# Optimization experiments

Hardware: AMD Instinct MI355X
Metric: run time of the kernel (lower is better)

Reference implementation:

```python
import jax, jax.numpy as jnp
import numpy as np

INPUT_SIZE = 1024
HIDDEN_SIZE = 1024
BATCH = 32
SEQ_LEN = 1024


def setup_inputs() -> dict:
    key = jax.random.key(0)
    k1, k2, k3, k4 = jax.random.split(key, 4)
    scale_x = 1.0 / np.sqrt(INPUT_SIZE)
    scale_h = 1.0 / np.sqrt(HIDDEN_SIZE)
    X = jax.random.normal(k1, (BATCH, SEQ_LEN, INPUT_SIZE), dtype=jnp.float32)
    W_xh = jax.random.normal(k2, (INPUT_SIZE, HIDDEN_SIZE), dtype=jnp.float32) * scale_x
    W_hh = jax.random.normal(k3, (HIDDEN_SIZE, HIDDEN_SIZE), dtype=jnp.float32) * scale_h
    b_h = jax.random.normal(k4, (HIDDEN_SIZE,), dtype=jnp.float32) * 0.01
    return {"X": X, "W_xh": W_xh, "W_hh": W_hh, "b_h": b_h}


def reference(X, W_xh, W_hh, b_h):
    # Elman RNN: H_t = tanh(X_t @ W_xh + H_{t-1} @ W_hh + b)
    B, S, _ = X.shape
    H0 = jnp.zeros((B, W_hh.shape[0]), dtype=X.dtype)
    # Precompute input projection for all timesteps in one big GEMM.
    Xp = jnp.einsum('bsi,ih->bsh', X, W_xh) + b_h  # [B, S, H]

    def step(H, xp_t):
        H_new = jnp.tanh(xp_t + H @ W_hh)
        return H_new, H_new

    H_last, outs = jax.lax.scan(step, H0, jnp.swapaxes(Xp, 0, 1))  # outs: [S, B, H]
    out = jnp.swapaxes(outs, 0, 1)  # [B, S, H]
    return out, H_last
```

## Files before the change

kernel.cpp:

```cpp
#include <hip/hip_runtime.h>
#include <hip/hip_bf16.h>
#include <math.h>


#define B_SZ 32
#define S_SZ 1024
#define H_SZ 1024
#define K_SZ 1024

#define BM 128
#define BN 128
#define BK 8

__global__ __launch_bounds__(256) void proj_gemm(
    const float* __restrict__ A,
    const float* __restrict__ Bm,
    const float* __restrict__ bias,
    float* __restrict__ C,
    int M, int N, int K)
{
    __shared__ float As[BK][BM];
    __shared__ float Bs[BK][BN];

    const int tid  = threadIdx.x;
    const int row0 = blockIdx.y * BM;
    const int col0 = blockIdx.x * BN;
    const int tx = tid & 15;
    const int ty = tid >> 4;
    const int mBase = ty * 8;
    const int nBase = tx * 8;

    float acc[8][8];
    #pragma unroll
    for (int i = 0; i < 8; ++i)
        #pragma unroll
        for (int j = 0; j < 8; ++j) acc[i][j] = 0.f;

    for (int k0 = 0; k0 < K; k0 += BK) {
        {
            const int r  = tid >> 1;
            const int kq = (tid & 1) * 4;
            const float4 av = *(const float4*)(&A[(size_t)(row0 + r) * K + k0 + kq]);
            As[kq + 0][r] = av.x;
            As[kq + 1][r] = av.y;
            As[kq + 2][r] = av.z;
            As[kq + 3][r] = av.w;
            const int kr = tid >> 5;
            const int cq = (tid & 31) * 4;
            *(float4*)(&Bs[kr][cq]) =
                *(const float4*)(&Bm[(size_t)(k0 + kr) * N + col0 + cq]);
        }
        __syncthreads();

        #pragma unroll
        for (int kk = 0; kk < BK; ++kk) {
            float a[8], b[8];
            *(float4*)&a[0] = *(const float4*)&As[kk][mBase];
            *(float4*)&a[4] = *(const float4*)&As[kk][mBase + 4];
            *(float4*)&b[0] = *(const float4*)&Bs[kk][nBase];
            *(float4*)&b[4] = *(const float4*)&Bs[kk][nBase + 4];
            #pragma unroll
            for (int i = 0; i < 8; ++i)
                #pragma unroll
                for (int j = 0; j < 8; ++j)
                    acc[i][j] += a[i] * b[j];
        }
        __syncthreads();
    }

    #pragma unroll
    for (int i = 0; i < 8; ++i) {
        const int r = row0 + mBase + i;
        #pragma unroll
        for (int jq = 0; jq < 8; jq += 4) {
            const int c = col0 + nBase + jq;
            const float4 bv = *(const float4*)(&bias[c]);
            float4 o;
            o.x = acc[i][jq + 0] + bv.x;
            o.y = acc[i][jq + 1] + bv.y;
            o.z = acc[i][jq + 2] + bv.z;
            o.w = acc[i][jq + 3] + bv.w;
            *(float4*)(&C[(size_t)r * N + c]) = o;
        }
    }
}

__global__ void init_cnt(unsigned int* __restrict__ cnt, int n) {
    int i = blockIdx.x * 256 + threadIdx.x;
    if (i < n) cnt[i] = 0u;
}

__global__ __launch_bounds__(512, 2) void rnn_persist(
    float* __restrict__ HS,
    const float* __restrict__ W,
    float* __restrict__ Hlast,
    unsigned int* __restrict__ cnt
    )
{
    const int g    = blockIdx.x & 7;
    const int c    = blockIdx.x >> 3;
    const int col0 = c * 32;
    const int b0   = g * 4;
    const int tid  = threadIdx.x;
    const int j    = tid & 31;
    const int seg  = tid >> 5;

    __shared__ __align__(16) float Hs[4][1024];
    __shared__ float red[8][4][32];

    float w[64];
    {
        const float* wp = W + (size_t)(seg * 64) * H_SZ + col0 + j;
        #pragma unroll
        for (int i = 0; i < 64; ++i) w[i] = wp[(size_t)i * H_SZ];
        #pragma unroll
        for (int i = 0; i < 64; ++i) asm volatile("" : "+v"(w[i]));
    }

    unsigned int* flag = cnt + g * S_SZ;

    for (int t = 0; t < S_SZ; ++t) {
        if (t > 0) {
            if (tid == 0) {
                while (__hip_atomic_load(flag + (t - 1), __ATOMIC_RELAXED,
                                         __HIP_MEMORY_SCOPE_AGENT) < 32u) {
                    __builtin_amdgcn_s_sleep(2);
                }
            }
            __syncthreads();

            #pragma unroll
            for (int ch = 0; ch < 4; ++ch) {
                const int f8 = tid + ch * 512;
                const int b  = f8 >> 9;
                const int qw = f8 & 511;
                const unsigned long long* src = (const unsigned long long*)
                    (&HS[((size_t)(b0 + b) * S_SZ + (t - 1)) * H_SZ]);
                const unsigned long long v8 = __hip_atomic_load(
                    &src[qw], __ATOMIC_RELAXED, __HIP_MEMORY_SCOPE_AGENT);
                *(unsigned long long*)(&Hs[b][qw * 2]) = v8;
            }
            __syncthreads();

            float acc[4];
            #pragma unroll
            for (int b = 0; b < 4; ++b) {
                const float4* hb = (const float4*)(&Hs[b][seg * 64]);
                float a = 0.f;
                #pragma unroll
                for (int q = 0; q < 16; ++q) {
                    const float4 h = hb[q];
                    a += h.x * w[4 * q + 0];
                    a += h.y * w[4 * q + 1];
                    a += h.z * w[4 * q + 2];
                    a += h.w * w[4 * q + 3];
                }
                acc[b] = a;
            }
            #pragma unroll
            for (int b = 0; b < 4; ++b) acc[b] += __shfl_xor(acc[b], 32);
            const int wv = tid >> 6;
            if ((tid & 63) < 32) {
                #pragma unroll
                for (int b = 0; b < 4; ++b) red[wv][b][j] = acc[b];
            }
            __syncthreads();
        }

        if (tid < 128) {
            const int b  = tid >> 5;
            const int jj = tid & 31;
            float s = 0.f;
            if (t > 0) {
                #pragma unroll
                for (int wv2 = 0; wv2 < 8; ++wv2) s += red[wv2][b][jj];
            }
            const size_t idx = ((size_t)(b0 + b) * S_SZ + t) * H_SZ + col0 + jj;
            const float v = tanhf(HS[idx] + s);
            __hip_atomic_store(&HS[idx], v, __ATOMIC_RELAXED,
                               __HIP_MEMORY_SCOPE_AGENT);
            if (t == S_SZ - 1)
                Hlast[(size_t)(b0 + b) * H_SZ + col0 + jj] = v;
        }

        __syncthreads();
        if (tid == 0) {
            __hip_atomic_fetch_add(flag + t, 1u, __ATOMIC_RELAXED,
                                   __HIP_MEMORY_SCOPE_AGENT);
        }
    }
}

extern "C" void kernel_launch(void* const* d_in, const int* in_sizes, int n_in,
                              void* d_out, int out_size, void* d_ws, size_t ws_size,
                              hipStream_t stream) {
    const float* X    = (const float*)d_in[0];
    const float* W_xh = (const float*)d_in[1];
    const float* W_hh = (const float*)d_in[2];
    const float* b_h  = (const float*)d_in[3];
    float* out = (float*)d_out;
    float* Hlast = out + (size_t)B_SZ * S_SZ * H_SZ;
    unsigned int* cnt = (unsigned int*)d_ws;

    init_cnt<<<(8 * S_SZ + 255) / 256, 256, 0, stream>>>(cnt, 8 * S_SZ);

    dim3 gridA(H_SZ / BN, (B_SZ * S_SZ) / BM);
    proj_gemm<<<gridA, 256, 0, stream>>>(X, W_xh, b_h, out,
                                         B_SZ * S_SZ, H_SZ, K_SZ);

    rnn_persist<<<256, 512, 0, stream>>>(out, W_hh, Hlast, cnt);
}
```

Measured before the change: 4.714 ms.

## Replace shared step counter with per-block flags polled by all threads

Replaces the per-timestep shared atomic counter with one monotonically increasing flag per producer block. Each thread polls only the flag of the block that wrote the slice it loads, so the leading thread spin plus block barrier before loading the previous hidden state goes away. The change also prefetches the input-projection values at the start of each step, uses an exp-based fast tanh, and drops one block barrier by publishing the flag right after a vmcnt wait in the writer threads. In exchange it takes on memory-ordering risk, since it relies on relaxed atomics plus s_waitcnt for visibility, and the fast tanh is slightly less accurate.

```diff
diff --git a/kernel.cpp b/kernel.cpp
--- a/kernel.cpp
+++ b/kernel.cpp
@@ -1,5 +1,4 @@
 #include <hip/hip_runtime.h>
-#include <hip/hip_bf16.h>
 #include <math.h>
 
 
@@ -88,6 +87,12 @@
 __global__ void init_cnt(unsigned int* __restrict__ cnt, int n) {
     int i = blockIdx.x * 256 + threadIdx.x;
     if (i < n) cnt[i] = 0u;
+}
+
+__device__ __forceinline__ float fast_tanh(float x) {
+    const float cx = fminf(fmaxf(x, -15.f), 15.f);
+    const float e  = __expf(2.f * cx);
+    return __fdividef(e - 1.f, e + 1.f);
 }
 
 __global__ __launch_bounds__(512, 2) void rnn_persist(
@@ -117,29 +122,42 @@
         for (int i = 0; i < 64; ++i) asm volatile("" : "+v"(w[i]));
     }
 
-    unsigned int* flag = cnt + g * S_SZ;
+    unsigned int* gcnt  = cnt + g * 32;
+    unsigned int* mycnt = gcnt + c;
+
+    const int sb = tid >> 7;
+    const int sr = tid & 127;
+    const unsigned int* pollp = gcnt + (sr >> 2);
+
+    const int je = tid & 31;
+    const int be = (tid >> 5) & 1;
 
     for (int t = 0; t < S_SZ; ++t) {
+        float xp0 = 0.f, xp1 = 0.f;
+        if (tid < 64) {
+            xp0 = HS[((size_t)(b0 + be)     * S_SZ + t) * H_SZ + col0 + je];
+            xp1 = HS[((size_t)(b0 + be + 2) * S_SZ + t) * H_SZ + col0 + je];
+        }
+
         if (t > 0) {
-            if (tid == 0) {
-                while (__hip_atomic_load(flag + (t - 1), __ATOMIC_RELAXED,
-                                         __HIP_MEMORY_SCOPE_AGENT) < 32u) {
-                    __builtin_amdgcn_s_sleep(2);
-                }
-            }
-            __syncthreads();
-
-            #pragma unroll
-            for (int ch = 0; ch < 4; ++ch) {
-                const int f8 = tid + ch * 512;
-                const int b  = f8 >> 9;
-                const int qw = f8 & 511;
-                const unsigned long long* src = (const unsigned long long*)
-                    (&HS[((size_t)(b0 + b) * S_SZ + (t - 1)) * H_SZ]);
-                const unsigned long long v8 = __hip_atomic_load(
-                    &src[qw], __ATOMIC_RELAXED, __HIP_MEMORY_SCOPE_AGENT);
-                *(unsigned long long*)(&Hs[b][qw * 2]) = v8;
-            }
+            unsigned int v;
+            do {
+                v = __hip_atomic_load(pollp, __ATOMIC_RELAXED,
+                                      __HIP_MEMORY_SCOPE_AGENT);
+            } while (v < (unsigned int)t);
+
+            const unsigned long long* src = (const unsigned long long*)
+                (&HS[((size_t)(b0 + sb) * S_SZ + (t - 1)) * H_SZ]);
+            const unsigned long long v0 = __hip_atomic_load(
+                src + 4 * sr + 0, __ATOMIC_RELAXED, __HIP_MEMORY_SCOPE_AGENT);
+            const unsigned long long v1 = __hip_atomic_load(
+                src + 4 * sr + 1, __ATOMIC_RELAXED, __HIP_MEMORY_SCOPE_AGENT);
+            const unsigned long long v2 = __hip_atomic_load(
+                src + 4 * sr + 2, __ATOMIC_RELAXED, __HIP_MEMORY_SCOPE_AGENT);
+            const unsigned long long v3 = __hip_atomic_load(
+                src + 4 * sr + 3, __ATOMIC_RELAXED, __HIP_MEMORY_SCOPE_AGENT);
+            unsigned long long* dst = (unsigned long long*)(&Hs[sb][8 * sr]);
+            dst[0] = v0; dst[1] = v1; dst[2] = v2; dst[3] = v3;
             __syncthreads();
 
             float acc[4];
@@ -164,29 +182,35 @@
                 #pragma unroll
                 for (int b = 0; b < 4; ++b) red[wv][b][j] = acc[b];
             }
-            __syncthreads();
-        }
-
-        if (tid < 128) {
-            const int b  = tid >> 5;
-            const int jj = tid & 31;
-            float s = 0.f;
+        }
+        __syncthreads();
+
+        if (tid < 64) {
+            float s0 = 0.f, s1 = 0.f;
             if (t > 0) {
                 #pragma unroll
-                for (int wv2 = 0; wv2 < 8; ++wv2) s += red[wv2][b][jj];
-            }
-            const size_t idx = ((size_t)(b0 + b) * S_SZ + t) * H_SZ + col0 + jj;
-            const float v = tanhf(HS[idx] + s);
-            __hip_atomic_store(&HS[idx], v, __ATOMIC_RELAXED,
+                for (int wv2 = 0; wv2 < 8; ++wv2) {
+                    s0 += red[wv2][be][je];
+                    s1 += red[wv2][be + 2][je];
+                }
+            }
+            const float h0 = fast_tanh(xp0 + s0);
+            const float h1 = fast_tanh(xp1 + s1);
+            const size_t i0 = ((size_t)(b0 + be)     * S_SZ + t) * H_SZ + col0 + je;
+            const size_t i1 = ((size_t)(b0 + be + 2) * S_SZ + t) * H_SZ + col0 + je;
+            __hip_atomic_store((float*)&HS[i0], h0, __ATOMIC_RELAXED,
                                __HIP_MEMORY_SCOPE_AGENT);
-            if (t == S_SZ - 1)
-                Hlast[(size_t)(b0 + b) * H_SZ + col0 + jj] = v;
-        }
-
-        __syncthreads();
-        if (tid == 0) {
-            __hip_atomic_fetch_add(flag + t, 1u, __ATOMIC_RELAXED,
-                                   __HIP_MEMORY_SCOPE_AGENT);
+            __hip_atomic_store((float*)&HS[i1], h1, __ATOMIC_RELAXED,
+                               __HIP_MEMORY_SCOPE_AGENT);
+            if (t == S_SZ - 1) {
+                Hlast[(size_t)(b0 + be)     * H_SZ + col0 + je] = h0;
+                Hlast[(size_t)(b0 + be + 2) * H_SZ + col0 + je] = h1;
+            }
+            asm volatile("s_waitcnt vmcnt(0)" ::: "memory");
+            if (tid == 0) {
+                __hip_atomic_store(mycnt, (unsigned int)(t + 1),
+                                   __ATOMIC_RELAXED, __HIP_MEMORY_SCOPE_AGENT);
+            }
         }
     }
 }
@@ -202,7 +226,7 @@
     float* Hlast = out + (size_t)B_SZ * S_SZ * H_SZ;
     unsigned int* cnt = (unsigned int*)d_ws;
 
-    init_cnt<<<(8 * S_SZ + 255) / 256, 256, 0, stream>>>(cnt, 8 * S_SZ);
+    init_cnt<<<1, 256, 0, stream>>>(cnt, 8 * 32);
 
     dim3 gridA(H_SZ / BN, (B_SZ * S_SZ) / BM);
     proj_gemm<<<gridA, 256, 0, stream>>>(X, W_xh, b_h, out,
```

After: 5.376 ms. 1.14x slower.
